# Performance work log

Measured on AMD Instinct MI355X. Metric: run time of the kernel, lower is better.

The kernel has to match this reference:

```python
import jax, jax.numpy as jnp
import numpy as np

N_NODES = 50000
N_EDGES = 800000
IN_CH = 128
OUT_CH = 64
SELF_LOOP_W = 2.0  # improved=True in GCNConv


def setup_inputs() -> dict:
    key = jax.random.key(0)
    k1, k2, k3, k4 = jax.random.split(key, 4)
    x = jax.random.normal(k1, (N_NODES, IN_CH), dtype=jnp.float32)
    edge_index = jax.random.randint(k2, (2, N_EDGES), 0, N_NODES, dtype=jnp.int64)
    edge_weight = jax.random.uniform(k3, (N_EDGES,), dtype=jnp.float32)
    W = jax.random.normal(k4, (IN_CH, OUT_CH), dtype=jnp.float32) / np.sqrt(IN_CH)
    b = jnp.zeros((OUT_CH,), dtype=jnp.float32)
    return {"x": x, "edge_index": edge_index, "edge_weight": edge_weight, "W": W, "b": b}


def reference(x, edge_index, edge_weight, W, b):
    # Only the first GCNConv layer runs (the torch loop returns after k=0).
    N = x.shape[0]
    row, col = edge_index[0], edge_index[1]  # source, target

    # gcn_norm with add_self_loops=True, improved=True (fill value 2.0)
    loop_idx = jnp.arange(N, dtype=edge_index.dtype)
    row_f = jnp.concatenate([row, loop_idx])
    col_f = jnp.concatenate([col, loop_idx])
    ew_f = jnp.concatenate([edge_weight, jnp.full((N,), SELF_LOOP_W, dtype=edge_weight.dtype)])

    deg = jax.ops.segment_sum(ew_f, col_f, num_segments=N)          # [N]
    dinv = jnp.where(deg > 0, jax.lax.rsqrt(deg), 0.0)
    norm = dinv[row_f] * ew_f * dinv[col_f]                          # [E+N]

    # linear transform then normalized sparse aggregation
    xw = x @ W                                                       # [N, out]
    msg = norm[:, None] * xw[row_f]                                  # [E+N, out] gather
    out = jax.ops.segment_sum(msg, col_f, num_segments=N)           # [N, out] scatter-add
    return out + b
```

## Files before the change

### kernel.cpp

```cpp
#include <hip/hip_runtime.h>

constexpr int N    = 50000;
constexpr int E    = 800000;
constexpr int CIN  = 128;
constexpr int COUT = 64;
constexpr float SELF_LOOP_W = 2.0f;

constexpr int NB   = (N + 63) / 64;
constexpr int CAP  = 1536;
constexpr int EPB  = 4096;
constexpr int PBLK = (E + EPB - 1) / EPB;

typedef float          vfloat4  __attribute__((ext_vector_type(4)));
typedef int            vint2    __attribute__((ext_vector_type(2)));
typedef unsigned short vushort4 __attribute__((ext_vector_type(4)));

__device__ __forceinline__ unsigned short f2bf(float f) {
    unsigned int u = __float_as_uint(f);
    u += 0x7FFFu + ((u >> 16) & 1u);
    return (unsigned short)(u >> 16);
}
__device__ __forceinline__ float bf2f(unsigned short h) {
    return __uint_as_float(((unsigned int)h) << 16);
}

__global__ __launch_bounds__(512) void partition_kernel(const int* __restrict__ row,
                                                        const int* __restrict__ col,
                                                        const float* __restrict__ ew,
                                                        int* __restrict__ bcur,
                                                        vint2* __restrict__ pk) {
    __shared__ int lhist[NB];
    __shared__ int lbase[NB];
    const int t  = threadIdx.x;
    const int e0 = blockIdx.x * EPB;

    for (int i = t; i < NB; i += 512) lhist[i] = 0;
    __syncthreads();

    #pragma unroll
    for (int k = 0; k < EPB / 512; ++k) {
        int e = e0 + k * 512 + t;
        if (e < E) atomicAdd(&lhist[col[e] >> 6], 1);
    }
    __syncthreads();

    for (int i = t; i < NB; i += 512) {
        int h = lhist[i];
        if (h > 0) lbase[i] = i * CAP + atomicAdd(&bcur[i], h);
    }
    __syncthreads();
    for (int i = t; i < NB; i += 512) lhist[i] = 0;
    __syncthreads();

    #pragma unroll
    for (int k = 0; k < EPB / 512; ++k) {
        int e = e0 + k * 512 + t;
        if (e < E) {
            int c   = col[e];
            int bkt = c >> 6;
            int p = lbase[bkt] + atomicAdd(&lhist[bkt], 1);
            if (p < (bkt + 1) * CAP) {
                vint2 v;
                v.x = row[e] | ((c & 63) << 20);
                v.y = __float_as_int(ew[e]);
                pk[p] = v;
            }
        }
    }
}

__global__ __launch_bounds__(256) void xw_deg_kernel(const float* __restrict__ x,
                                                     const float* __restrict__ W,
                                                     const int* __restrict__ bcur,
                                                     const vint2* __restrict__ pk,
                                                     unsigned short* __restrict__ xwh,
                                                     float* __restrict__ dinv) {
    __shared__ __align__(16) float xs[64][132];
    __shared__ float ldeg[64];

    const int t    = threadIdx.x;
    const int b    = blockIdx.x;
    const int base = b * 64;

    #pragma unroll
    for (int i = 0; i < 8; ++i) {
        int f4  = i * 256 + t;
        int r   = f4 >> 5;
        int c4  = f4 & 31;
        int node = base + r;
        if (node >= N) node = N - 1;
        vfloat4 v = *(const vfloat4*)(x + (size_t)node * CIN + c4 * 4);
        *(vfloat4*)&xs[r][c4 * 4] = v;
    }
    if (t < 64) ldeg[t] = 0.f;
    __syncthreads();

    const int tc = t & 15;
    const int tn = t >> 4;

    float acc[4][4];
    #pragma unroll
    for (int i = 0; i < 4; ++i)
        #pragma unroll
        for (int j = 0; j < 4; ++j) acc[i][j] = 0.f;

    const float* Wp = W + tc * 4;
    #pragma unroll 8
    for (int k = 0; k < CIN; ++k) {
        vfloat4 bv = *(const vfloat4*)(Wp + (size_t)k * COUT);
        float a0 = xs[tn * 4 + 0][k];
        float a1 = xs[tn * 4 + 1][k];
        float a2 = xs[tn * 4 + 2][k];
        float a3 = xs[tn * 4 + 3][k];
        #pragma unroll
        for (int j = 0; j < 4; ++j) {
            acc[0][j] += a0 * bv[j];
            acc[1][j] += a1 * bv[j];
            acc[2][j] += a2 * bv[j];
            acc[3][j] += a3 * bv[j];
        }
    }

    #pragma unroll
    for (int i = 0; i < 4; ++i) {
        int node = base + tn * 4 + i;
        if (node >= N) continue;
        vushort4 hv;
        #pragma unroll
        for (int j = 0; j < 4; ++j) hv[j] = f2bf(acc[i][j]);
        *(vushort4*)(xwh + (size_t)node * COUT + tc * 4) = hv;
    }

    const int pbase = b * CAP;
    const int cnt   = min(bcur[b], CAP);
    for (int j = t; j < cnt; j += 256) {
        vint2 v = pk[pbase + j];
        atomicAdd(&ldeg[(v.x >> 20) & 63], __int_as_float(v.y));
    }
    __syncthreads();
    int node = base + t;
    if (t < 64 && node < N) dinv[node] = rsqrtf(SELF_LOOP_W + ldeg[t]);
}

__global__ __launch_bounds__(512) void aggregate_kernel(const int* __restrict__ bcur,
                                                        const vint2* __restrict__ pk,
                                                        const float* __restrict__ dinv,
                                                        const unsigned short* __restrict__ xwh,
                                                        const float* __restrict__ bias,
                                                        float* __restrict__ out) {
    __shared__ int   rawx[CAP];
    __shared__ float rawn[CAP];
    __shared__ int   s_r[CAP];
    __shared__ float s_n[CAP];
    __shared__ int   lhist[64], lofs[64], lcur[64];

    const int t    = threadIdx.x;
    const int lane = t & 63;
    const int wv   = t >> 6;
    const int b    = blockIdx.x;
    const int base = b * CAP;
    const int cnt  = min(bcur[b], CAP);

    if (t < 64) lhist[t] = 0;
    __syncthreads();

    for (int j = t; j < cnt; j += 512) {
        vint2 v = pk[base + j];
        rawx[j] = v.x;
        rawn[j] = __int_as_float(v.y) * dinv[v.x & 0xFFFFF];
        atomicAdd(&lhist[(v.x >> 20) & 63], 1);
    }
    __syncthreads();

    if (t < 64) {
        int v = lhist[t];
        int s = v;
        #pragma unroll
        for (int d = 1; d < 64; d <<= 1) {
            int u = __shfl_up(s, d);
            if (lane >= d) s += u;
        }
        lofs[t] = s - v;
        lcur[t] = s - v;
    }
    __syncthreads();

    for (int j = t; j < cnt; j += 512) {
        int xv = rawx[j];
        int p  = atomicAdd(&lcur[(xv >> 20) & 63], 1);
        s_r[p] = xv & 0xFFFFF;
        s_n[p] = rawn[j];
    }
    __syncthreads();

    const int q  = lane >> 4;
    const int c4 = lane & 15;

    for (int nd = wv; nd < 64; nd += 8) {
        int node = b * 64 + nd;
        if (node >= N) continue;
        int s0 = lofs[nd];
        int e0 = s0 + lhist[nd];

        float a0 = 0.f, a1 = 0.f, a2 = 0.f, a3 = 0.f;
        for (int i = s0; i < e0; i += 16) {
            int rr[4]; float nn[4]; vushort4 vv[4];
            #pragma unroll
            for (int u = 0; u < 4; ++u) {
                int j = i + 4 * u + q;
                bool ok = (j < e0);
                rr[u] = ok ? s_r[j] : s_r[s0];
                nn[u] = ok ? s_n[j] : 0.f;
            }
            #pragma unroll
            for (int u = 0; u < 4; ++u)
                vv[u] = *(const vushort4*)(xwh + (size_t)rr[u] * COUT + c4 * 4);
            #pragma unroll
            for (int u = 0; u < 4; ++u) {
                a0 += nn[u] * bf2f(vv[u][0]);
                a1 += nn[u] * bf2f(vv[u][1]);
                a2 += nn[u] * bf2f(vv[u][2]);
                a3 += nn[u] * bf2f(vv[u][3]);
            }
        }
        a0 += __shfl_xor(a0, 16); a0 += __shfl_xor(a0, 32);
        a1 += __shfl_xor(a1, 16); a1 += __shfl_xor(a1, 32);
        a2 += __shfl_xor(a2, 16); a2 += __shfl_xor(a2, 32);
        a3 += __shfl_xor(a3, 16); a3 += __shfl_xor(a3, 32);

        if (q == 0) {
            float dc = dinv[node];
            float s2 = SELF_LOOP_W * dc * dc;
            vushort4 sh = *(const vushort4*)(xwh + (size_t)node * COUT + c4 * 4);
            vfloat4  bv = *(const vfloat4*)(bias + c4 * 4);
            vfloat4  o;
            o[0] = dc * a0 + s2 * bf2f(sh[0]) + bv[0];
            o[1] = dc * a1 + s2 * bf2f(sh[1]) + bv[1];
            o[2] = dc * a2 + s2 * bf2f(sh[2]) + bv[2];
            o[3] = dc * a3 + s2 * bf2f(sh[3]) + bv[3];
            *(vfloat4*)(out + (size_t)node * COUT + c4 * 4) = o;
        }
    }
}

extern "C" void kernel_launch(void* const* d_in, const int* in_sizes, int n_in,
                              void* d_out, int out_size, void* d_ws, size_t ws_size,
                              hipStream_t stream) {
    const float* x  = (const float*)d_in[0];
    const int*   ei = (const int*)d_in[1];
    const float* ew = (const float*)d_in[2];
    const float* W  = (const float*)d_in[3];
    const float* b  = (const float*)d_in[4];
    float* out = (float*)d_out;

    unsigned short* xwh  = (unsigned short*)d_ws;
    float*          dinv = (float*)(xwh + (size_t)N * COUT);
    int*            bcur = (int*)(dinv + N);
    vint2*          pk   = (vint2*)(bcur + NB + 2);

    const int* rowp = ei;
    const int* colp = ei + E;

    hipMemsetAsync(bcur, 0, NB * sizeof(int), stream);
    partition_kernel<<<PBLK, 512, 0, stream>>>(rowp, colp, ew, bcur, pk);
    xw_deg_kernel   <<<NB, 256, 0, stream>>>(x, W, bcur, pk, xwh, dinv);
    aggregate_kernel<<<NB, 512, 0, stream>>>(bcur, pk, dinv, xwh, b, out);
}
```

Measured before the change: 146.5 us.

## Replace per-block counting sort with LDS atomic accumulation in aggregation

The aggregate kernel no longer histograms, prefix-scans and reorders each bucket's edges by target node. Each group of 8 threads instead handles one edge, loads 8 bf16 features with a single 16-byte gather, and atomically adds the weighted values into a padded 64x65 shared-memory accumulator. This removes two sync phases and the local sort, and lets all 512 threads gather in parallel rather than one wave per node. The cost is 8 LDS float atomics per thread per edge, with possible contention when edges share a target node.

```diff
diff --git a/kernel.cpp b/kernel.cpp
--- a/kernel.cpp
+++ b/kernel.cpp
@@ -14,6 +14,7 @@
 typedef float          vfloat4  __attribute__((ext_vector_type(4)));
 typedef int            vint2    __attribute__((ext_vector_type(2)));
 typedef unsigned short vushort4 __attribute__((ext_vector_type(4)));
+typedef unsigned short vushort8 __attribute__((ext_vector_type(8)));
 
 __device__ __forceinline__ unsigned short f2bf(float f) {
     unsigned int u = __float_as_uint(f);
@@ -148,98 +149,51 @@
                                                         const unsigned short* __restrict__ xwh,
                                                         const float* __restrict__ bias,
                                                         float* __restrict__ out) {
-    __shared__ int   rawx[CAP];
-    __shared__ float rawn[CAP];
-    __shared__ int   s_r[CAP];
-    __shared__ float s_n[CAP];
-    __shared__ int   lhist[64], lofs[64], lcur[64];
+    __shared__ float acc[64][65];
 
     const int t    = threadIdx.x;
-    const int lane = t & 63;
-    const int wv   = t >> 6;
     const int b    = blockIdx.x;
     const int base = b * CAP;
     const int cnt  = min(bcur[b], CAP);
 
-    if (t < 64) lhist[t] = 0;
-    __syncthreads();
-
-    for (int j = t; j < cnt; j += 512) {
-        vint2 v = pk[base + j];
-        rawx[j] = v.x;
-        rawn[j] = __int_as_float(v.y) * dinv[v.x & 0xFFFFF];
-        atomicAdd(&lhist[(v.x >> 20) & 63], 1);
-    }
-    __syncthreads();
-
-    if (t < 64) {
-        int v = lhist[t];
-        int s = v;
-        #pragma unroll
-        for (int d = 1; d < 64; d <<= 1) {
-            int u = __shfl_up(s, d);
-            if (lane >= d) s += u;
+    for (int i = t; i < 64 * 65; i += 512) ((float*)acc)[i] = 0.f;
+    __syncthreads();
+
+    const int o  = t & 7;
+    const int rq = t >> 3;
+
+    for (int j = rq; j < cnt; j += 64) {
+        vint2 v   = pk[base + j];
+        int   row = v.x & 0xFFFFF;
+        int   ln  = (v.x >> 20) & 63;
+        float nrm = __int_as_float(v.y) * dinv[row];
+        vushort8 hv = *(const vushort8*)(xwh + (size_t)row * COUT + o * 8);
+        float* ap = &acc[ln][o * 8];
+        #pragma unroll
+        for (int u = 0; u < 8; ++u)
+            atomicAdd(&ap[u], nrm * bf2f(hv[u]));
+    }
+    __syncthreads();
+
+    const int nd   = t >> 3;
+    const int node = b * 64 + nd;
+    if (node < N) {
+        float dc = dinv[node];
+        float s2 = SELF_LOOP_W * dc * dc;
+        const int c0 = o * 8;
+        vushort8 sh = *(const vushort8*)(xwh + (size_t)node * COUT + c0);
+        vfloat4 bv0 = *(const vfloat4*)(bias + c0);
+        vfloat4 bv1 = *(const vfloat4*)(bias + c0 + 4);
+        float res[8];
+        #pragma unroll
+        for (int u = 0; u < 8; ++u) {
+            float bb = (u < 4) ? bv0[u] : bv1[u - 4];
+            res[u] = dc * acc[nd][c0 + u] + s2 * bf2f(sh[u]) + bb;
         }
-        lofs[t] = s - v;
-        lcur[t] = s - v;
-    }
-    __syncthreads();
-
-    for (int j = t; j < cnt; j += 512) {
-        int xv = rawx[j];
-        int p  = atomicAdd(&lcur[(xv >> 20) & 63], 1);
-        s_r[p] = xv & 0xFFFFF;
-        s_n[p] = rawn[j];
-    }
-    __syncthreads();
-
-    const int q  = lane >> 4;
-    const int c4 = lane & 15;
-
-    for (int nd = wv; nd < 64; nd += 8) {
-        int node = b * 64 + nd;
-        if (node >= N) continue;
-        int s0 = lofs[nd];
-        int e0 = s0 + lhist[nd];
-
-        float a0 = 0.f, a1 = 0.f, a2 = 0.f, a3 = 0.f;
-        for (int i = s0; i < e0; i += 16) {
-            int rr[4]; float nn[4]; vushort4 vv[4];
-            #pragma unroll
-            for (int u = 0; u < 4; ++u) {
-                int j = i + 4 * u + q;
-                bool ok = (j < e0);
-                rr[u] = ok ? s_r[j] : s_r[s0];
-                nn[u] = ok ? s_n[j] : 0.f;
-            }
-            #pragma unroll
-            for (int u = 0; u < 4; ++u)
-                vv[u] = *(const vushort4*)(xwh + (size_t)rr[u] * COUT + c4 * 4);
-            #pragma unroll
-            for (int u = 0; u < 4; ++u) {
-                a0 += nn[u] * bf2f(vv[u][0]);
-                a1 += nn[u] * bf2f(vv[u][1]);
-                a2 += nn[u] * bf2f(vv[u][2]);
-                a3 += nn[u] * bf2f(vv[u][3]);
-            }
-        }
-        a0 += __shfl_xor(a0, 16); a0 += __shfl_xor(a0, 32);
-        a1 += __shfl_xor(a1, 16); a1 += __shfl_xor(a1, 32);
-        a2 += __shfl_xor(a2, 16); a2 += __shfl_xor(a2, 32);
-        a3 += __shfl_xor(a3, 16); a3 += __shfl_xor(a3, 32);
-
-        if (q == 0) {
-            float dc = dinv[node];
-            float s2 = SELF_LOOP_W * dc * dc;
-            vushort4 sh = *(const vushort4*)(xwh + (size_t)node * COUT + c4 * 4);
-            vfloat4  bv = *(const vfloat4*)(bias + c4 * 4);
-            vfloat4  o;
-            o[0] = dc * a0 + s2 * bf2f(sh[0]) + bv[0];
-            o[1] = dc * a1 + s2 * bf2f(sh[1]) + bv[1];
-            o[2] = dc * a2 + s2 * bf2f(sh[2]) + bv[2];
-            o[3] = dc * a3 + s2 * bf2f(sh[3]) + bv[3];
-            *(vfloat4*)(out + (size_t)node * COUT + c4 * 4) = o;
-        }
+        vfloat4 o0 = { res[0], res[1], res[2], res[3] };
+        vfloat4 o1 = { res[4], res[5], res[6], res[7] };
+        *(vfloat4*)(out + (size_t)node * COUT + c0)     = o0;
+        *(vfloat4*)(out + (size_t)node * COUT + c0 + 4) = o1;
     }
 }
 
```

After: 462.1 us. +215.4%, slower.
